# Kernel optimization log

Hardware: AMD Instinct MI355X
Metric: run time of the kernel (lower is better)

## Reference

```python
import jax, jax.numpy as jnp
import numpy as np

B, T, S, H = 8, 512, 1024, 2048
VOCAB = 32000
START_TEXT, END_TEXT, START_SPEECH, END_SPEECH, DEFAULT_SPEECH = 1, 2, 3, 4, 5
IGNORE = -100


def setup_inputs() -> dict:
    key = jax.random.key(0)
    k_sp, k_emb, k_pw = jax.random.split(key, 3)
    rng = np.random.RandomState(0)
    n = rng.randint(T // 2, T + 1, size=B)
    n[0] = T  # guarantee static max output length T + S - 1
    s = rng.randint(S // 2, S + 1, size=B)
    s[0] = S
    input_ids = rng.randint(10, VOCAB, size=(B, T)).astype(np.int32)
    labels = rng.randint(10, VOCAB, size=(B, T)).astype(np.int32)
    mask = np.zeros((B, T), dtype=bool)
    for i in range(B):
        mask[i, : n[i]] = True
        p = rng.randint(2, n[i] - 2)  # speech placeholder position
        input_ids[i, 0] = START_TEXT
        input_ids[i, n[i] - 1] = END_TEXT
        input_ids[i, p - 1] = START_SPEECH
        input_ids[i, p] = DEFAULT_SPEECH
        input_ids[i, p + 1] = END_SPEECH
        input_ids[i, n[i]:] = 0
    return {
        "speech_features": jax.random.normal(k_sp, (B, S, H), jnp.float32),
        "speech_feature_lens": jnp.asarray(s, jnp.int32),
        "inputs_embeds": jax.random.normal(k_emb, (B, T, H), jnp.float32),
        "input_ids": jnp.asarray(input_ids),
        "attention_mask": jnp.asarray(mask),
        "labels": jnp.asarray(labels),
        "prompt_weight": jax.random.normal(k_pw, (4, H), jnp.float32),
    }


def reference(speech_features, speech_feature_lens, inputs_embeds, input_ids,
              attention_mask, labels, prompt_weight):
    # Merge speech features into the token-embedding stream at the (unique)
    # DEFAULT_SPEECH placeholder, substitute prompt embeddings at the four
    # marker tokens, then left-pad everything (flip+pad+flip in the original).
    b, t, h = inputs_embeds.shape
    s_max = speech_features.shape[1]
    L = t + s_max - 1  # static max merged length
    valid = attention_mask  # [B,T] bool, contiguous ones from position 0
    n = valid.sum(-1).astype(jnp.int32)  # [B] valid text lengths

    # prompt-embedding substitution at the first occurrence of each marker
    pos_t = jnp.arange(t)
    emb = inputs_embeds
    for r, tid in enumerate((START_TEXT, END_TEXT, START_SPEECH, END_SPEECH)):
        m = (input_ids == tid) & valid  # [B,T]
        first = jnp.argmax(m, axis=-1)  # [B]
        sel = (pos_t[None, :] == first[:, None]) & m.any(-1)[:, None]
        emb = jnp.where(sel[..., None], prompt_weight[r], emb)

    p = jnp.argmax((input_ids == DEFAULT_SPEECH) & valid, axis=-1).astype(jnp.int32)  # [B]
    s = speech_feature_lens  # [B]
    out_len = n + s - 1  # placeholder token replaced by s speech frames

    # k = position inside the merged (unpadded) sequence; left padding of L-out_len
    k = jnp.arange(L)[None, :] - (L - out_len)[:, None]  # [B,L]
    in_speech = (k >= p[:, None]) & (k < (p + s)[:, None])
    valid_out = (k >= 0) & (k < out_len[:, None])
    text_idx = jnp.clip(jnp.where(k < p[:, None], k, k - s[:, None] + 1), 0, t - 1)
    sp_idx = jnp.clip(k - p[:, None], 0, s_max - 1)

    text_g = jnp.take_along_axis(emb, text_idx[..., None], axis=1)  # [B,L,H]
    sp_g = jnp.take_along_axis(speech_features, sp_idx[..., None], axis=1)  # [B,L,H]
    out_emb = jnp.where(valid_out[..., None],
                        jnp.where(in_speech[..., None], sp_g, text_g), 0.0)
    out_mask = valid_out  # [B,L] bool, True on the right-aligned valid region
    lbl_g = jnp.take_along_axis(labels, text_idx, axis=1)  # [B,L]
    out_lbl = jnp.where(valid_out & ~in_speech, lbl_g, IGNORE)
    return out_emb, out_mask, out_lbl
```

## Files before the change

kernel.cpp:

```cpp
#include <hip/hip_runtime.h>

#define BB 8
#define TT 512
#define SS 1024
#define HH 2048
#define LL (TT + SS - 1)
#define TOK_DEFAULT_SPEECH 5

__global__ __launch_bounds__(64) void scalars_kernel(
    const int* __restrict__ input_ids, int* __restrict__ ws)
{
    const int b = blockIdx.x;
    const int lane = threadIdx.x;
    const int* row = input_ids + b * TT;
    int cnt = 0;
    int p = 0;
    #pragma unroll
    for (int t = lane; t < TT; t += 64) {
        const int id = row[t];
        cnt += (id != 0);
        if (id == TOK_DEFAULT_SPEECH) p = t;
    }
    #pragma unroll
    for (int off = 32; off > 0; off >>= 1) {
        cnt += __shfl_down(cnt, off);
        const int po = __shfl_down(p, off);
        p = (po > p) ? po : p;
    }
    if (lane == 0) {
        ws[b * 2 + 0] = cnt;
        ws[b * 2 + 1] = p;
    }
}

__global__ __launch_bounds__(256) void merge_kernel(
    const float* __restrict__ speech,
    const int*   __restrict__ slens,
    const float* __restrict__ embeds,
    const int*   __restrict__ labels,
    const float* __restrict__ pw,
    const int*   __restrict__ ws,
    float*       __restrict__ out)
{
    const int l = blockIdx.x;
    const int b = blockIdx.y;
    const int n = ws[b * 2 + 0];
    const int p = ws[b * 2 + 1];
    const int s = slens[b];
    const int out_len = n + s - 1;
    const int k = l - (LL - out_len);

    const bool valid = (k >= 0) && (k < out_len);
    const bool in_sp = valid && (k >= p) && (k < p + s);

    const float* src = nullptr;
    float lbl = -100.0f;
    if (valid) {
        if (in_sp) {
            src = speech + ((size_t)(b * SS + (k - p))) * HH;
        } else {
            const int ti = (k < p) ? k : (k - s + 1);
            int r = -1;
            if (ti == 0)          r = 0;
            else if (ti == n - 1) r = 1;
            else if (ti == p - 1) r = 2;
            else if (ti == p + 1) r = 3;
            src = (r >= 0) ? (pw + (size_t)r * HH)
                           : (embeds + ((size_t)(b * TT + ti)) * HH);
            lbl = (float)labels[b * TT + ti];
        }
    }

    float* out_emb  = out + ((size_t)(b * LL + l)) * HH;
    float* out_mask = out + (size_t)BB * LL * HH;
    float* out_lbl  = out_mask + (size_t)BB * LL;

    const int tid = threadIdx.x;
    if (tid == 0) {
        out_mask[b * LL + l] = valid ? 1.0f : 0.0f;
        out_lbl [b * LL + l] = lbl;
    }

    float4* d4 = (float4*)out_emb;
    if (valid) {
        const float4* s4 = (const float4*)src;
        d4[tid]       = s4[tid];
        d4[tid + 256] = s4[tid + 256];
    } else {
        const float4 z = make_float4(0.f, 0.f, 0.f, 0.f);
        d4[tid]       = z;
        d4[tid + 256] = z;
    }
}

extern "C" void kernel_launch(void* const* d_in, const int* in_sizes, int n_in,
                              void* d_out, int out_size, void* d_ws, size_t ws_size,
                              hipStream_t stream)
{
    const float* speech = (const float*)d_in[0];
    const int*   slens  = (const int*)  d_in[1];
    const float* embeds = (const float*)d_in[2];
    const int*   ids    = (const int*)  d_in[3];
    const int*   labels = (const int*)  d_in[5];
    const float* pw     = (const float*)d_in[6];
    float* out = (float*)d_out;
    int*   ws  = (int*)d_ws;

    scalars_kernel<<<dim3(BB), dim3(64), 0, stream>>>(ids, ws);
    merge_kernel<<<dim3(LL, BB), dim3(256), 0, stream>>>(
        speech, slens, embeds, labels, pw, ws, out);
}
```

Before: 189.6 us.

## Fuse scalar scan into merge kernel, process four rows per block, nontemporal I/O

Removes the separate scalars kernel: each merge block now recomputes the valid length and speech placeholder position itself from the 512 input ids, using a block-wide reduction through shared memory. Each block copies four output rows instead of one so the redundant scan is amortised. Loads and stores for the large embedding and speech rows use nontemporal hints to avoid polluting cache. The cost is a small amount of extra id-reading and two barriers per block, in exchange for one fewer kernel launch and no serialising dependency between kernels.

```diff
diff --git a/kernel.cpp b/kernel.cpp
--- a/kernel.cpp
+++ b/kernel.cpp
@@ -5,91 +5,108 @@
 #define SS 1024
 #define HH 2048
 #define LL (TT + SS - 1)
+#define ROWS 4
 #define TOK_DEFAULT_SPEECH 5
 
-__global__ __launch_bounds__(64) void scalars_kernel(
-    const int* __restrict__ input_ids, int* __restrict__ ws)
+typedef float v4f __attribute__((ext_vector_type(4)));
+
+__global__ __launch_bounds__(256) void merge_kernel(
+    const float* __restrict__ speech,
+    const int*   __restrict__ slens,
+    const float* __restrict__ embeds,
+    const int*   __restrict__ ids,
+    const int*   __restrict__ labels,
+    const float* __restrict__ pw,
+    float*       __restrict__ out)
 {
-    const int b = blockIdx.x;
-    const int lane = threadIdx.x;
-    const int* row = input_ids + b * TT;
-    int cnt = 0;
+    const int b   = blockIdx.y;
+    const int l0  = blockIdx.x * ROWS;
+    const int tid = threadIdx.x;
+    const int lane = tid & 63;
+    const int wave = tid >> 6;
+
+    const int* row = ids + b * TT;
+    const int idA = row[tid];
+    const int idB = row[tid + 256];
+    int cnt = (idA != 0) + (idB != 0);
     int p = 0;
-    #pragma unroll
-    for (int t = lane; t < TT; t += 64) {
-        const int id = row[t];
-        cnt += (id != 0);
-        if (id == TOK_DEFAULT_SPEECH) p = t;
-    }
+    if (idA == TOK_DEFAULT_SPEECH) p = tid;
+    if (idB == TOK_DEFAULT_SPEECH) p = tid + 256;
     #pragma unroll
     for (int off = 32; off > 0; off >>= 1) {
         cnt += __shfl_down(cnt, off);
         const int po = __shfl_down(p, off);
         p = (po > p) ? po : p;
     }
-    if (lane == 0) {
-        ws[b * 2 + 0] = cnt;
-        ws[b * 2 + 1] = p;
+    __shared__ int scnt[4], spos[4], sh_np[2];
+    if (lane == 0) { scnt[wave] = cnt; spos[wave] = p; }
+    __syncthreads();
+    if (tid == 0) {
+        const int nn = scnt[0] + scnt[1] + scnt[2] + scnt[3];
+        int pp = spos[0];
+        pp = spos[1] > pp ? spos[1] : pp;
+        pp = spos[2] > pp ? spos[2] : pp;
+        pp = spos[3] > pp ? spos[3] : pp;
+        sh_np[0] = nn;
+        sh_np[1] = pp;
     }
-}
+    __syncthreads();
+    const int n  = sh_np[0];
+    const int pp = sh_np[1];
+    const int s  = slens[b];
+    const int out_len = n + s - 1;
 
-__global__ __launch_bounds__(256) void merge_kernel(
-    const float* __restrict__ speech,
-    const int*   __restrict__ slens,
-    const float* __restrict__ embeds,
-    const int*   __restrict__ labels,
-    const float* __restrict__ pw,
-    const int*   __restrict__ ws,
-    float*       __restrict__ out)
-{
-    const int l = blockIdx.x;
-    const int b = blockIdx.y;
-    const int n = ws[b * 2 + 0];
-    const int p = ws[b * 2 + 1];
-    const int s = slens[b];
-    const int out_len = n + s - 1;
-    const int k = l - (LL - out_len);
+    float* const out_mask = out + (size_t)BB * LL * HH;
+    float* const out_lbl  = out_mask + (size_t)BB * LL;
 
-    const bool valid = (k >= 0) && (k < out_len);
-    const bool in_sp = valid && (k >= p) && (k < p + s);
+    #pragma unroll
+    for (int r = 0; r < ROWS; ++r) {
+        const int l = l0 + r;
+        if (l >= LL) break;
 
-    const float* src = nullptr;
-    float lbl = -100.0f;
-    if (valid) {
-        if (in_sp) {
-            src = speech + ((size_t)(b * SS + (k - p))) * HH;
-        } else {
-            const int ti = (k < p) ? k : (k - s + 1);
-            int r = -1;
-            if (ti == 0)          r = 0;
-            else if (ti == n - 1) r = 1;
-            else if (ti == p - 1) r = 2;
-            else if (ti == p + 1) r = 3;
-            src = (r >= 0) ? (pw + (size_t)r * HH)
-                           : (embeds + ((size_t)(b * TT + ti)) * HH);
-            lbl = (float)labels[b * TT + ti];
+        const int k = l - (LL - out_len);
+        const bool valid = (k >= 0) && (k < out_len);
+        const bool in_sp = valid && (k >= pp) && (k < pp + s);
+
+        v4f v0 = (v4f)(0.f);
+        v4f v1 = (v4f)(0.f);
+        float lbl = -100.0f;
+
+        if (valid) {
+            if (in_sp) {
+                const v4f* s4 = (const v4f*)
+                    (speech + ((size_t)(b * SS + (k - pp))) * HH);
+                v0 = __builtin_nontemporal_load(s4 + tid);
+                v1 = __builtin_nontemporal_load(s4 + tid + 256);
+            } else {
+                const int ti = (k < pp) ? k : (k - s + 1);
+                int pr = -1;
+                if (ti == 0)           pr = 0;
+                else if (ti == n - 1)  pr = 1;
+                else if (ti == pp - 1) pr = 2;
+                else if (ti == pp + 1) pr = 3;
+                if (pr >= 0) {
+                    const v4f* s4 = (const v4f*)(pw + (size_t)pr * HH);
+                    v0 = s4[tid];
+                    v1 = s4[tid + 256];
+                } else {
+                    const v4f* s4 = (const v4f*)
+                        (embeds + ((size_t)(b * TT + ti)) * HH);
+                    v0 = __builtin_nontemporal_load(s4 + tid);
+                    v1 = __builtin_nontemporal_load(s4 + tid + 256);
+                }
+                lbl = (float)labels[b * TT + ti];
+            }
         }
-    }
 
-    float* out_emb  = out + ((size_t)(b * LL + l)) * HH;
-    float* out_mask = out + (size_t)BB * LL * HH;
-    float* out_lbl  = out_mask + (size_t)BB * LL;
+        v4f* d4 = (v4f*)(out + ((size_t)(b * LL + l)) * HH);
+        __builtin_nontemporal_store(v0, d4 + tid);
+        __builtin_nontemporal_store(v1, d4 + tid + 256);
 
-    const int tid = threadIdx.x;
-    if (tid == 0) {
-        out_mask[b * LL + l] = valid ? 1.0f : 0.0f;
-        out_lbl [b * LL + l] = lbl;
-    }
-
-    float4* d4 = (float4*)out_emb;
-    if (valid) {
-        const float4* s4 = (const float4*)src;
-        d4[tid]       = s4[tid];
-        d4[tid + 256] = s4[tid + 256];
-    } else {
-        const float4 z = make_float4(0.f, 0.f, 0.f, 0.f);
-        d4[tid]       = z;
-        d4[tid + 256] = z;
+        if (tid == 0) {
+            out_mask[b * LL + l] = valid ? 1.0f : 0.0f;
+            out_lbl [b * LL + l] = lbl;
+        }
     }
 }
 
@@ -104,9 +121,8 @@
     const int*   labels = (const int*)  d_in[5];
     const float* pw     = (const float*)d_in[6];
     float* out = (float*)d_out;
-    int*   ws  = (int*)d_ws;
 
-    scalars_kernel<<<dim3(BB), dim3(64), 0, stream>>>(ids, ws);
-    merge_kernel<<<dim3(LL, BB), dim3(256), 0, stream>>>(
-        speech, slens, embeds, labels, pw, ws, out);
+    const int gx = (LL + ROWS - 1) / ROWS;
+    merge_kernel<<<dim3(gx, BB), dim3(256), 0, stream>>>(
+        speech, slens, embeds, ids, labels, pw, out);
 }
```

New measurement: 182.5 us. 3.7% less time.
